# Kernel optimization log

Hardware: AMD Instinct MI355X
Metric: run time of the kernel (lower is better)

Reference implementation:

```python
import jax, jax.numpy as jnp
import numpy as np

N = 10000
E = 320000
IN_DIM = 256
HID = 128
HEADS = 3
NEG_SLOPE = 0.2
EPS = 1e-8


def setup_inputs() -> dict:
    key = jax.random.key(0)
    ks = jax.random.split(key, 12)
    rn = lambda k, s, sc=0.1: jax.random.normal(k, s, dtype=jnp.float32) * sc
    return {
        'x1': jax.random.normal(ks[0], (N, IN_DIM), dtype=jnp.float32),
        'edge_index1': jax.random.randint(ks[1], (2, E), 0, N, dtype=jnp.int64),
        'x2': jax.random.normal(ks[2], (N, IN_DIM), dtype=jnp.float32),
        'edge_index2': jax.random.randint(ks[3], (2, E), 0, N, dtype=jnp.int64),
        'W1': rn(ks[4], (IN_DIM, HEADS * HID)),
        'att_src1': rn(ks[5], (HEADS, HID)),
        'att_dst1': rn(ks[6], (HEADS, HID)),
        'b1': rn(ks[7], (HEADS * HID,)),
        'W2': rn(ks[8], (HEADS * HID, HID)),
        'att_src2': rn(ks[9], (1, HID)),
        'att_dst2': rn(ks[10], (1, HID)),
        'b2': rn(ks[11], (HID,)),
    }


def gat_conv(x, edge_index, W, a_src, a_dst, bias, heads, out_ch, concat):
    """PyG-style GATConv with add_self_loops=True."""
    n = x.shape[0]
    loops = jnp.arange(n, dtype=edge_index.dtype)
    ei = jnp.concatenate([edge_index, jnp.stack([loops, loops])], axis=1)
    src, dst = ei[0], ei[1]
    h = (x @ W).reshape(n, heads, out_ch)                    # [N,H,C]
    s = jnp.einsum('nhc,hc->nh', h, a_src)                    # alpha_src per node
    d = jnp.einsum('nhc,hc->nh', h, a_dst)                    # alpha_dst per node
    e = jax.nn.leaky_relu(s[src] + d[dst], NEG_SLOPE)         # [Etot,H]
    m = jax.ops.segment_max(e, dst, num_segments=n)           # segment softmax (stable)
    ex = jnp.exp(e - m[dst])
    denom = jax.ops.segment_sum(ex, dst, num_segments=n)
    alpha = ex / denom[dst]                                   # [Etot,H]
    out = jax.ops.segment_sum(h[src] * alpha[:, :, None], dst, num_segments=n)
    out = out.reshape(n, heads * out_ch) if concat else out.mean(axis=1)
    return out + bias, (ei, alpha)


def _branch(x, ei, W1, as1, ad1, b1, W2, as2, ad2, b2):
    e1, (ei_sl, alpha1) = gat_conv(x, ei, W1, as1, ad1, b1, HEADS, HID, True)
    e1 = jax.nn.relu(e1)
    e2, _ = gat_conv(e1, ei, W2, as2, ad2, b2, 1, HID, False)
    # _graph_pooling
    attn_val = alpha1.mean(axis=1)                            # [Etot]
    node_attn = jax.ops.segment_sum(attn_val, ei_sl[1], num_segments=x.shape[0])
    weighted = e2 * node_attn[:, None]
    pooled = jnp.concatenate([weighted.mean(axis=0), e2.mean(axis=0)])  # [2*HID]
    return pooled, alpha1


def reference(x1, edge_index1, x2, edge_index2, W1, att_src1, att_dst1, b1,
              W2, att_src2, att_dst2, b2):
    g1, alpha1 = _branch(x1, edge_index1, W1, att_src1, att_dst1, b1,
                         W2, att_src2, att_dst2, b2)
    g2, alpha2 = _branch(x2, edge_index2, W1, att_src1, att_dst1, b1,
                         W2, att_src2, att_dst2, b2)
    n1 = jnp.maximum(jnp.linalg.norm(g1), EPS)
    n2 = jnp.maximum(jnp.linalg.norm(g2), EPS)
    sim = jnp.dot(g1, g2) / (n1 * n2)
    return sim, alpha1, alpha2
```

## Files before the change

kernel.cpp:

```cpp
#include <hip/hip_runtime.h>
#include <hip/hip_bf16.h>
#include <cstdint>
#include <cstddef>

#define INDIM 256
#define NEG 0.2f

typedef __attribute__((ext_vector_type(8))) short short8v;
typedef __attribute__((ext_vector_type(4))) float f32x4;
typedef __attribute__((ext_vector_type(2))) float f32x2;

__device__ __forceinline__ unsigned short f2bf(float x) {
  __hip_bfloat16 b = __float2bfloat16(x);
  return __builtin_bit_cast(unsigned short, b);
}

__device__ __forceinline__ unsigned char f2fp8(float v) {
  int packed = __builtin_amdgcn_cvt_pk_fp8_f32(v, v, 0, false);
  return (unsigned char)(packed & 0xff);
}

__device__ __forceinline__ float lrelu(float v) { return v > 0.f ? v : NEG * v; }

__global__ void wprep_kernel(const float* __restrict__ W1, __hip_bfloat16* __restrict__ W1t,
                             const float* __restrict__ W2, __hip_bfloat16* __restrict__ W2t) {
  int idx = blockIdx.x * blockDim.x + threadIdx.x;
  const int T1 = 256 * 384;
  if (idx < T1) {
    int k = idx / 384, c = idx - k * 384;
    W1t[(size_t)c * 256 + k] = __float2bfloat16(W1[idx]);
  } else {
    int i = idx - T1;
    if (i < 384 * 128) {
      int k = i / 128, c = i - k * 128;
      W2t[(size_t)c * 384 + k] = __float2bfloat16(W2[i]);
    }
  }
}

template<int K, bool ABF16>
__global__ __launch_bounds__(256) void mfma_gemm(const void* __restrict__ A0,
                                                 const void* __restrict__ A1, int Nsplit,
                                                 const __hip_bfloat16* __restrict__ Wt,
                                                 float* __restrict__ Y,
                                                 unsigned char* __restrict__ Yc,
                                                 int M, int NC) {
  __shared__ short As[64][40];
  __shared__ short Bs[128][40];
  const int tid = threadIdx.x;
  const int row0 = blockIdx.x * 64;
  const int col0 = blockIdx.y * 128;
  const int l = tid & 63, w = tid >> 6;
  const int wr = w >> 1, wc = w & 1;
  const int lr = l & 15, lk = (l >> 4) * 8;

  f32x4 acc[2][4];
#pragma unroll
  for (int m = 0; m < 2; ++m)
#pragma unroll
    for (int n = 0; n < 4; ++n) acc[m][n] = {0.f, 0.f, 0.f, 0.f};

  for (int k0 = 0; k0 < K; k0 += 32) {
    __syncthreads();
    {
      int r = tid >> 2, kq = (tid & 3) * 8;
      int gr = row0 + r;
      short8v av = {0, 0, 0, 0, 0, 0, 0, 0};
      if (gr < M) {
        const void* Ab = (gr < Nsplit) ? A0 : A1;
        int lrow = (gr < Nsplit) ? gr : gr - Nsplit;
        if (ABF16) {
          av = *(const short8v*)((const short*)Ab + (size_t)lrow * K + k0 + kq);
        } else {
          const float* ap = (const float*)Ab + (size_t)lrow * K + k0 + kq;
          float4 u = *(const float4*)ap;
          float4 v = *(const float4*)(ap + 4);
          av = short8v{(short)f2bf(u.x), (short)f2bf(u.y), (short)f2bf(u.z), (short)f2bf(u.w),
                       (short)f2bf(v.x), (short)f2bf(v.y), (short)f2bf(v.z), (short)f2bf(v.w)};
        }
      }
      *(short8v*)&As[r][kq] = av;
    }
    {
      int c = tid >> 1, kq = (tid & 1) * 8;
      const short* wp = (const short*)Wt + (size_t)(col0 + c) * K + k0 + kq;
      *(short8v*)&Bs[c][kq]      = *(const short8v*)wp;
      *(short8v*)&Bs[c][kq + 16] = *(const short8v*)(wp + 16);
    }
    __syncthreads();
    short8v a[2], b[4];
#pragma unroll
    for (int m = 0; m < 2; ++m) a[m] = *(short8v*)&As[wr * 32 + m * 16 + lr][lk];
#pragma unroll
    for (int n = 0; n < 4; ++n) b[n] = *(short8v*)&Bs[wc * 64 + n * 16 + lr][lk];
#pragma unroll
    for (int m = 0; m < 2; ++m)
#pragma unroll
      for (int n = 0; n < 4; ++n)
        acc[m][n] = __builtin_amdgcn_mfma_f32_16x16x32_bf16(a[m], b[n], acc[m][n], 0, 0, 0);
  }
#pragma unroll
  for (int m = 0; m < 2; ++m) {
    int rbase = row0 + wr * 32 + m * 16 + (l >> 4) * 4;
#pragma unroll
    for (int n = 0; n < 4; ++n) {
      int col = col0 + wc * 64 + n * 16 + lr;
#pragma unroll
      for (int q = 0; q < 4; ++q) {
        int row = rbase + q;
        if (row < M) {
          float v = acc[m][n][q];
          Y[(size_t)row * NC + col] = v;
          Yc[(size_t)row * NC + col] = f2fp8(v);
        }
      }
    }
  }
}

__global__ __launch_bounds__(256) void sd_kernel(const float* __restrict__ H,
                                                 const float* __restrict__ As,
                                                 const float* __restrict__ Ad,
                                                 float* __restrict__ S, float* __restrict__ D,
                                                 int NB, int NH) {
  int w = blockIdx.x * 4 + (threadIdx.x >> 6);
  if (w >= NB) return;
  int lane = threadIdx.x & 63;
  int h = w % NH;
  float2 hv = reinterpret_cast<const float2*>(H + (size_t)w * 128)[lane];
  float2 as = reinterpret_cast<const float2*>(As + h * 128)[lane];
  float2 ad = reinterpret_cast<const float2*>(Ad + h * 128)[lane];
  float vs = hv.x * as.x + hv.y * as.y;
  float vd = hv.x * ad.x + hv.y * ad.y;
#pragma unroll
  for (int o = 32; o; o >>= 1) { vs += __shfl_down(vs, o); vd += __shfl_down(vd, o); }
  if (lane == 0) { S[w] = vs; D[w] = vd; }
}

__global__ void deg_kernel(const int* __restrict__ ed1, const int* __restrict__ ed2,
                           int E, int Etot, int N, int* __restrict__ deg) {
  int idx = blockIdx.x * blockDim.x + threadIdx.x;
  if (idx >= 2 * Etot) return;
  int br = idx >= Etot;
  int el = idx - br * Etot;
  const int* ed = br ? ed2 : ed1;
  int dn = ((el < E) ? ed[el] : (el - E)) + br * N;
  atomicAdd(&deg[dn], 1);
}

__global__ __launch_bounds__(1024) void scan_kernel(const int* __restrict__ deg,
                                                    int* __restrict__ rowptr,
                                                    int* __restrict__ cursor, int n) {
  __shared__ int wsum[16];
  int t = threadIdx.x, lane = t & 63, wid = t >> 6;
  int start = t * 20;
  int v[20];
  int s = 0;
#pragma unroll
  for (int k = 0; k < 20; ++k) {
    int i = start + k;
    int d = (i < n) ? deg[i] : 0;
    s += d;
    v[k] = s;
  }
  int x = s;
#pragma unroll
  for (int o = 1; o < 64; o <<= 1) {
    int tm = __shfl_up(x, o);
    if (lane >= o) x += tm;
  }
  if (lane == 63) wsum[wid] = x;
  __syncthreads();
  if (wid == 0) {
    int wv = (lane < 16) ? wsum[lane] : 0;
#pragma unroll
    for (int o = 1; o < 16; o <<= 1) {
      int tm = __shfl_up(wv, o);
      if (lane >= o) wv += tm;
    }
    if (lane < 16) wsum[lane] = wv;
  }
  __syncthreads();
  int excl = (x - s) + (wid ? wsum[wid - 1] : 0);
  if (t == 0) rowptr[0] = 0;
#pragma unroll
  for (int k = 0; k < 20; ++k) {
    int i = start + k;
    if (i < n) {
      rowptr[i + 1] = excl + v[k];
      cursor[i] = excl + (k ? v[k - 1] : 0);
    }
  }
}

__global__ void fill_kernel(const int* __restrict__ es1, const int* __restrict__ ed1,
                            const int* __restrict__ es2, const int* __restrict__ ed2,
                            const float* __restrict__ S1, const float* __restrict__ D1,
                            int E, int Etot, int N, int* __restrict__ cursor,
                            int* __restrict__ csr_src, int* __restrict__ csr_dst,
                            float4* __restrict__ w4) {
  int idx = blockIdx.x * blockDim.x + threadIdx.x;
  if (idx >= 2 * Etot) return;
  int br = idx >= Etot;
  int el = idx - br * Etot;
  const int* es = br ? es2 : es1;
  const int* ed = br ? ed2 : ed1;
  int sn, dn;
  if (el < E) { sn = es[el]; dn = ed[el]; } else { sn = dn = el - E; }
  sn += br * N; dn += br * N;
  int pos = atomicAdd(&cursor[dn], 1);
  csr_src[pos] = sn;
  csr_dst[pos] = dn;
  float4 w;
  w.x = __expf(lrelu(S1[sn * 3]     + D1[dn * 3]));
  w.y = __expf(lrelu(S1[sn * 3 + 1] + D1[dn * 3 + 1]));
  w.z = __expf(lrelu(S1[sn * 3 + 2] + D1[dn * 3 + 2]));
  w.w = __int_as_float(br * Etot + el);
  w4[pos] = w;
}

__global__ void w2prep_kernel(const int* __restrict__ csr_src, const int* __restrict__ csr_dst,
                              const float* __restrict__ S2, const float* __restrict__ D2,
                              int total, float* __restrict__ w2) {
  int pos = blockIdx.x * blockDim.x + threadIdx.x;
  if (pos >= total) return;
  w2[pos] = __expf(lrelu(S2[csr_src[pos]] + D2[csr_dst[pos]]));
}

__global__ __launch_bounds__(192) void agg1_kernel(const unsigned char* __restrict__ h1c,
                                                   const int* __restrict__ rowptr,
                                                   const int* __restrict__ csr_src,
                                                   const float4* __restrict__ w4,
                                                   const float* __restrict__ b1,
                                                   __hip_bfloat16* __restrict__ e1b,
                                                   float* __restrict__ out) {
  __shared__ int lsrc[192];
  __shared__ float la[3][192];
  __shared__ float red[3][3];
  __shared__ float inv_s[3];
  const unsigned int* H4 = reinterpret_cast<const unsigned int*>(h1c);
  int n = blockIdx.x;
  int j = threadIdx.x;
  int wid = j >> 6, lane = j & 63;
  int half = (j >= 96) ? 1 : 0;
  int t = j - half * 96;
  int head = t >> 5;
  int p0 = rowptr[n], p1 = rowptr[n + 1];

  float dp0 = 0.f, dp1 = 0.f, dp2 = 0.f;
  float acc[4] = {0.f, 0.f, 0.f, 0.f};
  for (int base = p0; base < p1; base += 192) {
    int cnt = min(192, p1 - base);
    __syncthreads();
    if (j < cnt) {
      lsrc[j] = csr_src[base + j];
      float4 w = w4[base + j];
      la[0][j] = w.x; la[1][j] = w.y; la[2][j] = w.z;
      dp0 += w.x; dp1 += w.y; dp2 += w.z;
    }
    __syncthreads();
    int i = half;
    for (; i + 14 < cnt; i += 16) {
      unsigned int hv[8];
      float av[8];
#pragma unroll
      for (int u = 0; u < 8; ++u) {
        int e = i + 2 * u;
        int sn = lsrc[e];
        av[u] = la[head][e];
        hv[u] = H4[(size_t)sn * 96 + t];
      }
#pragma unroll
      for (int u = 0; u < 8; ++u) {
        f32x2 f0 = __builtin_amdgcn_cvt_pk_f32_fp8((int)hv[u], false);
        f32x2 f1 = __builtin_amdgcn_cvt_pk_f32_fp8((int)hv[u], true);
        acc[0] = fmaf(av[u], f0.x, acc[0]);
        acc[1] = fmaf(av[u], f0.y, acc[1]);
        acc[2] = fmaf(av[u], f1.x, acc[2]);
        acc[3] = fmaf(av[u], f1.y, acc[3]);
      }
    }
    for (; i < cnt; i += 2) {
      int sn = lsrc[i];
      float a = la[head][i];
      unsigned int hv = H4[(size_t)sn * 96 + t];
      f32x2 f0 = __builtin_amdgcn_cvt_pk_f32_fp8((int)hv, false);
      f32x2 f1 = __builtin_amdgcn_cvt_pk_f32_fp8((int)hv, true);
      acc[0] = fmaf(a, f0.x, acc[0]);
      acc[1] = fmaf(a, f0.y, acc[1]);
      acc[2] = fmaf(a, f1.x, acc[2]);
      acc[3] = fmaf(a, f1.y, acc[3]);
    }
  }
  __syncthreads();
  float* racc = &la[0][0];
  if (half == 1) {
    racc[t * 4 + 0] = acc[0]; racc[t * 4 + 1] = acc[1];
    racc[t * 4 + 2] = acc[2]; racc[t * 4 + 3] = acc[3];
  }
  __syncthreads();
  if (half == 0) {
    acc[0] += racc[t * 4 + 0]; acc[1] += racc[t * 4 + 1];
    acc[2] += racc[t * 4 + 2]; acc[3] += racc[t * 4 + 3];
  }
#pragma unroll
  for (int o = 32; o; o >>= 1) {
    dp0 += __shfl_down(dp0, o); dp1 += __shfl_down(dp1, o); dp2 += __shfl_down(dp2, o);
  }
  if (lane == 0) { red[wid][0] = dp0; red[wid][1] = dp1; red[wid][2] = dp2; }
  __syncthreads();
  if (j == 0) {
    inv_s[0] = 1.f / (red[0][0] + red[1][0] + red[2][0]);
    inv_s[1] = 1.f / (red[0][1] + red[1][1] + red[2][1]);
    inv_s[2] = 1.f / (red[0][2] + red[1][2] + red[2][2]);
  }
  __syncthreads();
  float i0 = inv_s[0], i1 = inv_s[1], i2 = inv_s[2];
  if (half == 0) {
    float inv = inv_s[head];
    float4 bb = *reinterpret_cast<const float4*>(b1 + 4 * t);
    float v0 = acc[0] * inv + bb.x;
    float v1 = acc[1] * inv + bb.y;
    float v2 = acc[2] * inv + bb.z;
    float v3 = acc[3] * inv + bb.w;
    v0 = v0 > 0.f ? v0 : 0.f; v1 = v1 > 0.f ? v1 : 0.f;
    v2 = v2 > 0.f ? v2 : 0.f; v3 = v3 > 0.f ? v3 : 0.f;
    uint2 st;
    st.x = (unsigned int)f2bf(v0) | ((unsigned int)f2bf(v1) << 16);
    st.y = (unsigned int)f2bf(v2) | ((unsigned int)f2bf(v3) << 16);
    *reinterpret_cast<uint2*>(reinterpret_cast<unsigned short*>(e1b) + (size_t)n * 384 + 4 * t) = st;
  }
  for (int p = p0 + j; p < p1; p += 192) {
    float4 w = w4[p];
    int eid = __float_as_int(w.w);
    float* ao = out + 1 + (size_t)eid * 3;
    ao[0] = w.x * i0;
    ao[1] = w.y * i1;
    ao[2] = w.z * i2;
  }
}

__global__ __launch_bounds__(64) void agg2_kernel(const unsigned char* __restrict__ h2c,
                                                  const float* __restrict__ w2,
                                                  const int* __restrict__ rowptr,
                                                  const int* __restrict__ csr_src,
                                                  const float* __restrict__ b2,
                                                  float* __restrict__ e2out) {
  __shared__ int lsrc[256];
  __shared__ float la[256];
  const unsigned int* H4 = reinterpret_cast<const unsigned int*>(h2c);
  int n = blockIdx.x;
  int lane = threadIdx.x;
  int half = lane >> 5, t = lane & 31;
  int p0 = rowptr[n], p1 = rowptr[n + 1];

  float dpart = 0.f;
  float acc[4] = {0.f, 0.f, 0.f, 0.f};
  for (int base = p0; base < p1; base += 256) {
    int cnt = min(256, p1 - base);
    __syncthreads();
    for (int i = lane; i < cnt; i += 64) {
      lsrc[i] = csr_src[base + i];
      float ex = w2[base + i];
      la[i] = ex;
      dpart += ex;
    }
    __syncthreads();
    int i = half;
    for (; i + 14 < cnt; i += 16) {
      unsigned int hv[8];
      float av[8];
#pragma unroll
      for (int u = 0; u < 8; ++u) {
        int e = i + 2 * u;
        int sn = lsrc[e];
        av[u] = la[e];
        hv[u] = H4[(size_t)sn * 32 + t];
      }
#pragma unroll
      for (int u = 0; u < 8; ++u) {
        f32x2 f0 = __builtin_amdgcn_cvt_pk_f32_fp8((int)hv[u], false);
        f32x2 f1 = __builtin_amdgcn_cvt_pk_f32_fp8((int)hv[u], true);
        acc[0] = fmaf(av[u], f0.x, acc[0]);
        acc[1] = fmaf(av[u], f0.y, acc[1]);
        acc[2] = fmaf(av[u], f1.x, acc[2]);
        acc[3] = fmaf(av[u], f1.y, acc[3]);
      }
    }
    for (; i < cnt; i += 2) {
      int sn = lsrc[i];
      float a = la[i];
      unsigned int hv = H4[(size_t)sn * 32 + t];
      f32x2 f0 = __builtin_amdgcn_cvt_pk_f32_fp8((int)hv, false);
      f32x2 f1 = __builtin_amdgcn_cvt_pk_f32_fp8((int)hv, true);
      acc[0] = fmaf(a, f0.x, acc[0]);
      acc[1] = fmaf(a, f0.y, acc[1]);
      acc[2] = fmaf(a, f1.x, acc[2]);
      acc[3] = fmaf(a, f1.y, acc[3]);
    }
  }
#pragma unroll
  for (int k = 0; k < 4; ++k) acc[k] += __shfl_xor(acc[k], 32);
#pragma unroll
  for (int o = 32; o; o >>= 1) dpart += __shfl_down(dpart, o);
  float invden = 1.f / __shfl(dpart, 0);
  if (half == 0) {
    float4 bb = *reinterpret_cast<const float4*>(b2 + 4 * t);
    float4 ov;
    ov.x = acc[0] * invden + bb.x;
    ov.y = acc[1] * invden + bb.y;
    ov.z = acc[2] * invden + bb.z;
    ov.w = acc[3] * invden + bb.w;
    *reinterpret_cast<float4*>(e2out + (size_t)n * 128 + 4 * t) = ov;
  }
}

__global__ __launch_bounds__(128) void pool_kernel(const float* __restrict__ e2,
                                                   float* __restrict__ g, int N, float invN) {
  int c = threadIdx.x;
  int br = blockIdx.y;
  int r0 = br * N + blockIdx.x * 128;
  int r1 = min(r0 + 128, br * N + N);
  float acc = 0.f;
  for (int n = r0; n < r1; ++n) acc += e2[(size_t)n * 128 + c];
  acc *= invN;
  float* gb = g + (size_t)br * 256;
  atomicAdd(&gb[c], acc);
  atomicAdd(&gb[128 + c], acc);
}

__global__ __launch_bounds__(256) void sim_kernel(const float* __restrict__ g1,
                                                  const float* __restrict__ g2,
                                                  float* __restrict__ out) {
  int t = threadIdx.x;
  float a = g1[t], b = g2[t];
  __shared__ float sd[256], s1[256], s2[256];
  sd[t] = a * b; s1[t] = a * a; s2[t] = b * b;
  __syncthreads();
  for (int ofs = 128; ofs; ofs >>= 1) {
    if (t < ofs) { sd[t] += sd[t + ofs]; s1[t] += s1[t + ofs]; s2[t] += s2[t + ofs]; }
    __syncthreads();
  }
  if (t == 0) {
    float n1 = fmaxf(sqrtf(s1[0]), 1e-8f);
    float n2 = fmaxf(sqrtf(s2[0]), 1e-8f);
    out[0] = sd[0] / (n1 * n2);
  }
}

extern "C" void kernel_launch(void* const* d_in, const int* in_sizes, int n_in,
                              void* d_out, int out_size, void* d_ws, size_t ws_size,
                              hipStream_t stream) {
  const int N = in_sizes[0] / INDIM;
  const int E = in_sizes[1] / 2;
  const int Etot = E + N;
  const int N2 = 2 * N;

  const float* x1  = (const float*)d_in[0];
  const int*   ei1 = (const int*)d_in[1];
  const float* x2  = (const float*)d_in[2];
  const int*   ei2 = (const int*)d_in[3];
  const float* W1  = (const float*)d_in[4];
  const float* as1 = (const float*)d_in[5];
  const float* ad1 = (const float*)d_in[6];
  const float* b1  = (const float*)d_in[7];
  const float* W2  = (const float*)d_in[8];
  const float* as2 = (const float*)d_in[9];
  const float* ad2 = (const float*)d_in[10];
  const float* b2  = (const float*)d_in[11];
  float* out = (float*)d_out;
  const int* es1 = ei1, *ed1 = ei1 + E;
  const int* es2 = ei2, *ed2 = ei2 + E;

  char* p = (char*)d_ws;
  auto alloc = [&](size_t bytes) -> char* {
    char* q = p;
    p += (bytes + 255) & ~(size_t)255;
    return q;
  };
  float* h1          = (float*)alloc((size_t)N2 * 384 * 4);
  unsigned char* h1c = (unsigned char*)alloc((size_t)N2 * 384);
  __hip_bfloat16* e1b = (__hip_bfloat16*)alloc((size_t)N2 * 384 * 2);
  float* h2          = (float*)alloc((size_t)N2 * 128 * 4);
  unsigned char* h2c = (unsigned char*)alloc((size_t)N2 * 128);
  float* e2          = (float*)alloc((size_t)N2 * 128 * 4);
  __hip_bfloat16* W1t = (__hip_bfloat16*)alloc((size_t)256 * 384 * 2);
  __hip_bfloat16* W2t = (__hip_bfloat16*)alloc((size_t)384 * 128 * 2);
  float* s1v  = (float*)alloc((size_t)N2 * 3 * 4);
  float* d1v  = (float*)alloc((size_t)N2 * 3 * 4);
  float* s2v  = (float*)alloc((size_t)N2 * 4);
  float* d2v  = (float*)alloc((size_t)N2 * 4);
  float* g    = (float*)alloc(512 * 4);
  int* deg     = (int*)alloc((size_t)N2 * 4);
  int* rowptr  = (int*)alloc((size_t)(N2 + 1) * 4);
  int* cursor  = (int*)alloc((size_t)N2 * 4);
  int* csr_src = (int*)alloc((size_t)2 * Etot * 4);
  int* csr_dst = (int*)alloc((size_t)2 * Etot * 4);
  float4* w4   = (float4*)alloc((size_t)2 * Etot * 16);
  float* w2    = (float*)alloc((size_t)2 * Etot * 4);

  const int EB = 256;
  const int egrid2 = (2 * Etot + EB - 1) / EB;
  const int gmx = (N2 + 63) / 64;

  hipMemsetAsync(g, 0, 512 * 4, stream);
  hipMemsetAsync(deg, 0, (size_t)N2 * 4, stream);
  wprep_kernel<<<(256 * 384 + 384 * 128 + 255) / 256, 256, 0, stream>>>(W1, W1t, W2, W2t);

  deg_kernel<<<egrid2, EB, 0, stream>>>(ed1, ed2, E, Etot, N, deg);
  mfma_gemm<256, false><<<dim3(gmx, 3), 256, 0, stream>>>(x1, x2, N, W1t, h1, h1c, N2, 384);
  sd_kernel<<<(N2 * 3 + 3) / 4, 256, 0, stream>>>(h1, as1, ad1, s1v, d1v, N2 * 3, 3);
  scan_kernel<<<1, 1024, 0, stream>>>(deg, rowptr, cursor, N2);
  fill_kernel<<<egrid2, EB, 0, stream>>>(es1, ed1, es2, ed2, s1v, d1v, E, Etot, N,
                                         cursor, csr_src, csr_dst, w4);

  agg1_kernel<<<N2, 192, 0, stream>>>(h1c, rowptr, csr_src, w4, b1, e1b, out);

  mfma_gemm<384, true><<<dim3(gmx, 1), 256, 0, stream>>>(e1b, e1b, N2, W2t, h2, h2c, N2, 128);
  sd_kernel<<<(N2 + 3) / 4, 256, 0, stream>>>(h2, as2, ad2, s2v, d2v, N2, 1);
  w2prep_kernel<<<egrid2, EB, 0, stream>>>(csr_src, csr_dst, s2v, d2v, 2 * Etot, w2);
  agg2_kernel<<<N2, 64, 0, stream>>>(h2c, w2, rowptr, csr_src, b2, e2);

  pool_kernel<<<dim3((N + 127) / 128, 2), 128, 0, stream>>>(e2, g, N, 1.f / (float)N);
  sim_kernel<<<1, 256, 0, stream>>>(g, g + 256, out);
}
```

Baseline: 261.9 us.

## Fuse attention-score dot products into GEMM epilogue and pack two nodes per agg2 block

The per-head source and destination attention dot products now run in the MFMA GEMM epilogue. They use cross-lane shuffles and a shared-memory combine of the two column warps, so the fp32 h1 and h2 buffers are no longer written and the separate sd_kernel launches are gone. agg2 now runs two wavefronts per block, each handling its own node with private LDS slices, which drops the block-wide barriers. Pooling now deduplicates the identical halves of the pooled vector: since weighted and plain means match, each half is stored once and the similarity uses 128 elements, which gives the same cosine. This removes fp32 store traffic and launches at the cost of a heavier GEMM epilogue.

```diff
diff --git a/kernel.cpp b/kernel.cpp
--- a/kernel.cpp
+++ b/kernel.cpp
@@ -38,15 +38,19 @@
   }
 }
 
-template<int K, bool ABF16>
+template<int K, bool ABF16, int NH>
 __global__ __launch_bounds__(256) void mfma_gemm(const void* __restrict__ A0,
                                                  const void* __restrict__ A1, int Nsplit,
                                                  const __hip_bfloat16* __restrict__ Wt,
-                                                 float* __restrict__ Y,
+                                                 const float* __restrict__ att_s,
+                                                 const float* __restrict__ att_d,
                                                  unsigned char* __restrict__ Yc,
+                                                 float* __restrict__ So,
+                                                 float* __restrict__ Do,
                                                  int M, int NC) {
   __shared__ short As[64][40];
   __shared__ short Bs[128][40];
+  __shared__ float sred[2][64];
   const int tid = threadIdx.x;
   const int row0 = blockIdx.x * 64;
   const int col0 = blockIdx.y * 128;
@@ -108,33 +112,65 @@
 #pragma unroll
       for (int q = 0; q < 4; ++q) {
         int row = rbase + q;
+        if (row < M) Yc[(size_t)row * NC + col] = f2fp8(acc[m][n][q]);
+      }
+    }
+  }
+  float asv[4], adv[4];
+#pragma unroll
+  for (int n = 0; n < 4; ++n) {
+    int col = col0 + wc * 64 + n * 16 + lr;
+    asv[n] = att_s[col];
+    adv[n] = att_d[col];
+  }
+  float ps[2][4], pd[2][4];
+#pragma unroll
+  for (int m = 0; m < 2; ++m)
+#pragma unroll
+    for (int q = 0; q < 4; ++q) {
+      float s = 0.f, d = 0.f;
+#pragma unroll
+      for (int n = 0; n < 4; ++n) {
+        s = fmaf(acc[m][n][q], asv[n], s);
+        d = fmaf(acc[m][n][q], adv[n], d);
+      }
+      ps[m][q] = s; pd[m][q] = d;
+    }
+#pragma unroll
+  for (int o = 1; o < 16; o <<= 1) {
+#pragma unroll
+    for (int m = 0; m < 2; ++m)
+#pragma unroll
+      for (int q = 0; q < 4; ++q) {
+        ps[m][q] += __shfl_xor(ps[m][q], o);
+        pd[m][q] += __shfl_xor(pd[m][q], o);
+      }
+  }
+  __syncthreads();
+  if (wc == 1 && lr == 0) {
+#pragma unroll
+    for (int m = 0; m < 2; ++m)
+#pragma unroll
+      for (int q = 0; q < 4; ++q) {
+        int rl = wr * 32 + m * 16 + (l >> 4) * 4 + q;
+        sred[0][rl] = ps[m][q];
+        sred[1][rl] = pd[m][q];
+      }
+  }
+  __syncthreads();
+  if (wc == 0 && lr == 0) {
+#pragma unroll
+    for (int m = 0; m < 2; ++m)
+#pragma unroll
+      for (int q = 0; q < 4; ++q) {
+        int rl = wr * 32 + m * 16 + (l >> 4) * 4 + q;
+        int row = row0 + rl;
         if (row < M) {
-          float v = acc[m][n][q];
-          Y[(size_t)row * NC + col] = v;
-          Yc[(size_t)row * NC + col] = f2fp8(v);
+          So[(size_t)row * NH + blockIdx.y] = ps[m][q] + sred[0][rl];
+          Do[(size_t)row * NH + blockIdx.y] = pd[m][q] + sred[1][rl];
         }
       }
-    }
-  }
-}
-
-__global__ __launch_bounds__(256) void sd_kernel(const float* __restrict__ H,
-                                                 const float* __restrict__ As,
-                                                 const float* __restrict__ Ad,
-                                                 float* __restrict__ S, float* __restrict__ D,
-                                                 int NB, int NH) {
-  int w = blockIdx.x * 4 + (threadIdx.x >> 6);
-  if (w >= NB) return;
-  int lane = threadIdx.x & 63;
-  int h = w % NH;
-  float2 hv = reinterpret_cast<const float2*>(H + (size_t)w * 128)[lane];
-  float2 as = reinterpret_cast<const float2*>(As + h * 128)[lane];
-  float2 ad = reinterpret_cast<const float2*>(Ad + h * 128)[lane];
-  float vs = hv.x * as.x + hv.y * as.y;
-  float vd = hv.x * ad.x + hv.y * ad.y;
-#pragma unroll
-  for (int o = 32; o; o >>= 1) { vs += __shfl_down(vs, o); vd += __shfl_down(vd, o); }
-  if (lane == 0) { S[w] = vs; D[w] = vd; }
+  }
 }
 
 __global__ void deg_kernel(const int* __restrict__ ed1, const int* __restrict__ ed2,
@@ -340,17 +376,19 @@
   }
 }
 
-__global__ __launch_bounds__(64) void agg2_kernel(const unsigned char* __restrict__ h2c,
-                                                  const float* __restrict__ w2,
-                                                  const int* __restrict__ rowptr,
-                                                  const int* __restrict__ csr_src,
-                                                  const float* __restrict__ b2,
-                                                  float* __restrict__ e2out) {
-  __shared__ int lsrc[256];
-  __shared__ float la[256];
+__global__ __launch_bounds__(128) void agg2_kernel(const unsigned char* __restrict__ h2c,
+                                                   const float* __restrict__ w2,
+                                                   const int* __restrict__ rowptr,
+                                                   const int* __restrict__ csr_src,
+                                                   const float* __restrict__ b2,
+                                                   float* __restrict__ e2out, int N2) {
+  __shared__ int lsrc[2][256];
+  __shared__ float la[2][256];
   const unsigned int* H4 = reinterpret_cast<const unsigned int*>(h2c);
-  int n = blockIdx.x;
-  int lane = threadIdx.x;
+  int wv = threadIdx.x >> 6;
+  int n = blockIdx.x * 2 + wv;
+  if (n >= N2) return;
+  int lane = threadIdx.x & 63;
   int half = lane >> 5, t = lane & 31;
   int p0 = rowptr[n], p1 = rowptr[n + 1];
 
@@ -358,14 +396,12 @@
   float acc[4] = {0.f, 0.f, 0.f, 0.f};
   for (int base = p0; base < p1; base += 256) {
     int cnt = min(256, p1 - base);
-    __syncthreads();
     for (int i = lane; i < cnt; i += 64) {
-      lsrc[i] = csr_src[base + i];
+      lsrc[wv][i] = csr_src[base + i];
       float ex = w2[base + i];
-      la[i] = ex;
+      la[wv][i] = ex;
       dpart += ex;
     }
-    __syncthreads();
     int i = half;
     for (; i + 14 < cnt; i += 16) {
       unsigned int hv[8];
@@ -373,8 +409,8 @@
 #pragma unroll
       for (int u = 0; u < 8; ++u) {
         int e = i + 2 * u;
-        int sn = lsrc[e];
-        av[u] = la[e];
+        int sn = lsrc[wv][e];
+        av[u] = la[wv][e];
         hv[u] = H4[(size_t)sn * 32 + t];
       }
 #pragma unroll
@@ -388,8 +424,8 @@
       }
     }
     for (; i < cnt; i += 2) {
-      int sn = lsrc[i];
-      float a = la[i];
+      int sn = lsrc[wv][i];
+      float a = la[wv][i];
       unsigned int hv = H4[(size_t)sn * 32 + t];
       f32x2 f0 = __builtin_amdgcn_cvt_pk_f32_fp8((int)hv, false);
       f32x2 f1 = __builtin_amdgcn_cvt_pk_f32_fp8((int)hv, true);
@@ -423,21 +459,18 @@
   int r1 = min(r0 + 128, br * N + N);
   float acc = 0.f;
   for (int n = r0; n < r1; ++n) acc += e2[(size_t)n * 128 + c];
-  acc *= invN;
-  float* gb = g + (size_t)br * 256;
-  atomicAdd(&gb[c], acc);
-  atomicAdd(&gb[128 + c], acc);
-}
-
-__global__ __launch_bounds__(256) void sim_kernel(const float* __restrict__ g1,
+  atomicAdd(&g[br * 128 + c], acc * invN);
+}
+
+__global__ __launch_bounds__(128) void sim_kernel(const float* __restrict__ g1,
                                                   const float* __restrict__ g2,
                                                   float* __restrict__ out) {
   int t = threadIdx.x;
   float a = g1[t], b = g2[t];
-  __shared__ float sd[256], s1[256], s2[256];
+  __shared__ float sd[128], s1[128], s2[128];
   sd[t] = a * b; s1[t] = a * a; s2[t] = b * b;
   __syncthreads();
-  for (int ofs = 128; ofs; ofs >>= 1) {
+  for (int ofs = 64; ofs; ofs >>= 1) {
     if (t < ofs) { sd[t] += sd[t + ofs]; s1[t] += s1[t + ofs]; s2[t] += s2[t + ofs]; }
     __syncthreads();
   }
@@ -478,10 +511,8 @@
     p += (bytes + 255) & ~(size_t)255;
     return q;
   };
-  float* h1          = (float*)alloc((size_t)N2 * 384 * 4);
   unsigned char* h1c = (unsigned char*)alloc((size_t)N2 * 384);
   __hip_bfloat16* e1b = (__hip_bfloat16*)alloc((size_t)N2 * 384 * 2);
-  float* h2          = (float*)alloc((size_t)N2 * 128 * 4);
   unsigned char* h2c = (unsigned char*)alloc((size_t)N2 * 128);
   float* e2          = (float*)alloc((size_t)N2 * 128 * 4);
   __hip_bfloat16* W1t = (__hip_bfloat16*)alloc((size_t)256 * 384 * 2);
@@ -490,7 +521,7 @@
   float* d1v  = (float*)alloc((size_t)N2 * 3 * 4);
   float* s2v  = (float*)alloc((size_t)N2 * 4);
   float* d2v  = (float*)alloc((size_t)N2 * 4);
-  float* g    = (float*)alloc(512 * 4);
+  float* g    = (float*)alloc(256 * 4);
   int* deg     = (int*)alloc((size_t)N2 * 4);
   int* rowptr  = (int*)alloc((size_t)(N2 + 1) * 4);
   int* cursor  = (int*)alloc((size_t)N2 * 4);
@@ -503,24 +534,24 @@
   const int egrid2 = (2 * Etot + EB - 1) / EB;
   const int gmx = (N2 + 63) / 64;
 
-  hipMemsetAsync(g, 0, 512 * 4, stream);
+  hipMemsetAsync(g, 0, 256 * 4, stream);
   hipMemsetAsync(deg, 0, (size_t)N2 * 4, stream);
   wprep_kernel<<<(256 * 384 + 384 * 128 + 255) / 256, 256, 0, stream>>>(W1, W1t, W2, W2t);
 
   deg_kernel<<<egrid2, EB, 0, stream>>>(ed1, ed2, E, Etot, N, deg);
-  mfma_gemm<256, false><<<dim3(gmx, 3), 256, 0, stream>>>(x1, x2, N, W1t, h1, h1c, N2, 384);
-  sd_kernel<<<(N2 * 3 + 3) / 4, 256, 0, stream>>>(h1, as1, ad1, s1v, d1v, N2 * 3, 3);
+  mfma_gemm<256, false, 3><<<dim3(gmx, 3), 256, 0, stream>>>(x1, x2, N, W1t, as1, ad1,
+                                                             h1c, s1v, d1v, N2, 384);
   scan_kernel<<<1, 1024, 0, stream>>>(deg, rowptr, cursor, N2);
   fill_kernel<<<egrid2, EB, 0, stream>>>(es1, ed1, es2, ed2, s1v, d1v, E, Etot, N,
                                          cursor, csr_src, csr_dst, w4);
 
   agg1_kernel<<<N2, 192, 0, stream>>>(h1c, rowptr, csr_src, w4, b1, e1b, out);
 
-  mfma_gemm<384, true><<<dim3(gmx, 1), 256, 0, stream>>>(e1b, e1b, N2, W2t, h2, h2c, N2, 128);
-  sd_kernel<<<(N2 + 3) / 4, 256, 0, stream>>>(h2, as2, ad2, s2v, d2v, N2, 1);
+  mfma_gemm<384, true, 1><<<dim3(gmx, 1), 256, 0, stream>>>(e1b, e1b, N2, W2t, as2, ad2,
+                                                            h2c, s2v, d2v, N2, 128);
   w2prep_kernel<<<egrid2, EB, 0, stream>>>(csr_src, csr_dst, s2v, d2v, 2 * Etot, w2);
-  agg2_kernel<<<N2, 64, 0, stream>>>(h2c, w2, rowptr, csr_src, b2, e2);
+  agg2_kernel<<<(N2 + 1) / 2, 128, 0, stream>>>(h2c, w2, rowptr, csr_src, b2, e2, N2);
 
   pool_kernel<<<dim3((N + 127) / 128, 2), 128, 0, stream>>>(e2, g, N, 1.f / (float)N);
-  sim_kernel<<<1, 256, 0, stream>>>(g, g + 256, out);
-}
+  sim_kernel<<<1, 128, 0, stream>>>(g, g + 128, out);
+}
```

New measurement: 248.9 us. -5.0%, faster.
